# Optimization experiments

Hardware: AMD Instinct MI355X
Metric: run time of the kernel (lower is better)

## Reference

```python
import jax, jax.numpy as jnp
import numpy as np

N, L, C = 4, 1024, 512   # batch, frames, channels (in_channels == mdl_channels)
H = 16                   # heads
D = C // H               # head dim
S = 16                   # number of segments for bi
EPS_PN = 1e-5            # MaskPowerNorm / GroupScaling eps


def setup_inputs() -> dict:
    key = jax.random.key(0)
    ks = jax.random.split(key, 8)
    x = jax.random.normal(ks[0], (N, L, C), jnp.float32)
    bi = jnp.sort(jax.random.randint(ks[1], (L,), 0, S)).astype(jnp.int64)
    w_qkv = jax.random.normal(ks[2], (3 * C, C), jnp.float32) * 0.02
    w_beta = jax.random.normal(ks[3], (1, 3 * C), jnp.float32) * 0.02
    w1 = jax.random.normal(ks[4], (C, C), jnp.float32) * 0.02
    b1 = jnp.zeros((C,), jnp.float32)
    w2 = jax.random.normal(ks[5], (C, C), jnp.float32) * 0.02
    b2 = jnp.zeros((C,), jnp.float32)
    pn1_w = jnp.ones((C,), jnp.float32)
    pn1_b = jnp.zeros((C,), jnp.float32)
    pn1_phi = jnp.ones((C,), jnp.float32)
    pn2_w = jnp.ones((C,), jnp.float32)
    pn2_b = jnp.zeros((C,), jnp.float32)
    pn2_phi = jnp.ones((C,), jnp.float32)
    return dict(x=x, bi=bi, w_qkv=w_qkv, w_beta=w_beta, w1=w1, b1=b1, w2=w2,
                b2=b2, pn1_w=pn1_w, pn1_b=pn1_b, pn1_phi=pn1_phi,
                pn2_w=pn2_w, pn2_b=pn2_b, pn2_phi=pn2_phi)


def power_norm(x, weight, bias, running_phi):
    # MaskPowerNorm (eval): GroupScaling1D over H channel groups, then
    # x / sqrt(running_phi + eps) * weight + bias
    n, l, c = x.shape
    cg = c // H
    g = x.reshape(n, l, H, cg)
    m2 = jnp.mean(g * g, axis=-1, keepdims=True)
    gs = (g / jnp.sqrt(m2 + EPS_PN)).reshape(n, l, c)
    return gs / jnp.sqrt(running_phi + EPS_PN) * weight + bias


def reference(x, bi, w_qkv, w_beta, w1, b1, w2, b2,
              pn1_w, pn1_b, pn1_phi, pn2_w, pn2_b, pn2_phi):
    n, l, c = x.shape
    d = c // H
    # QKV projection (bias=False)
    qkv = x @ w_qkv.T                                  # (n, l, 3c)
    q, k, v = jnp.split(qkv, 3, axis=-1)
    q = q.reshape(n, l, H, d)
    k = k.reshape(n, l, H, d)
    v = v.reshape(n, l, H, d)
    # elu feature map on temperature-scaled q, k
    temp = d ** (-0.25)
    phi = lambda t: jax.nn.elu(t * temp) + 1.0
    q = phi(q).transpose(0, 2, 1, 3)                   # (n, h, l, d)
    k = phi(k).transpose(0, 2, 1, 3)                   # (n, h, l, d)
    vt = v.transpose(0, 2, 1, 3)                       # (n, h, l, d)
    # per-position outer products k v^T : (n, h, l, d, d)
    kv = k[..., :, None] * vt[..., None, :]
    # scatter_sum over frames into S segments, then gather back per frame
    kv_seg = jnp.zeros((n, H, S, d, d), kv.dtype).at[:, :, bi].add(kv)
    kv_g = kv_seg[:, :, bi]                            # (n, h, l, d, d)
    k_seg = jnp.zeros((n, H, S, d), k.dtype).at[:, :, bi].add(k)
    k_g = k_seg[:, :, bi]                              # (n, h, l, d)
    z = 1.0 / jnp.sum(q * k_g, axis=-1)                # (n, h, l)
    v_out = jnp.einsum('nhld,nhldm->nhlm', q, kv_g) * z[..., None]
    t = v_out.transpose(0, 2, 1, 3).reshape(n, l, c)   # (n, l, c)
    # AddNorm with beta gate (dropout is identity in eval)
    beta = jax.nn.sigmoid(jnp.concatenate([t, x, t - x], axis=-1) @ w_beta.T)
    x1 = power_norm(beta * x + (1.0 - beta) * t, pn1_w, pn1_b, pn1_phi)
    # FFN (exact GELU) + AddNorm (no beta)
    ff = jax.nn.gelu(x1 @ w1.T + b1, approximate=False) @ w2.T + b2
    return power_norm(ff + x1, pn2_w, pn2_b, pn2_phi)
```

## Files before the change

### kernel.cpp

```cpp
#include <hip/hip_runtime.h>
#include <math.h>

#define NB 4
#define LB 1024
#define CB 512
#define HH 16
#define DD 32
#define SS 16
#define NL (NB*LB)
#define C3 (3*CB)

typedef __attribute__((ext_vector_type(8))) short short8;
typedef __attribute__((ext_vector_type(4))) float f32x4;

__device__ __forceinline__ unsigned short f2bf_rn(float f) {
  unsigned u = __builtin_bit_cast(unsigned, f);
  unsigned r = u + 0x7FFFu + ((u >> 16) & 1u);
  return (unsigned short)(r >> 16);
}
__device__ __forceinline__ float bf2f(unsigned short h) {
  unsigned u = ((unsigned)h) << 16;
  return __builtin_bit_cast(float, u);
}

__device__ __forceinline__ int lower_bound_i32(const int* a, int n, int v) {
  int lo = 0, hi = n;
  while (lo < hi) { int mid = (lo + hi) >> 1; if (a[mid] < v) lo = mid + 1; else hi = mid; }
  return lo;
}

template<int MODE, int BN>
__global__ __launch_bounds__(256) void gemm_mfma(
    const float* __restrict__ A, const float* __restrict__ B, float* __restrict__ Co,
    int M, int Nn, int K,
    const float* __restrict__ bias, const float* __restrict__ res)
{
  constexpr int NJ = BN / 32;
  __shared__ short8 Ah8[4*128], Al8[4*128];
  __shared__ short8 Bh8[4*BN],  Bl8[4*BN];
  const int tid  = threadIdx.x;
  const int lane = tid & 63, wave = tid >> 6;
  const int wm = wave >> 1, wn = wave & 1;
  const int l15 = lane & 15, l4 = lane >> 4;
  const int bm = blockIdx.x * 128, bn = blockIdx.y * BN;

  f32x4 acc[4][NJ];
  #pragma unroll
  for (int i = 0; i < 4; ++i)
    #pragma unroll
    for (int j = 0; j < NJ; ++j)
      acc[i][j] = {0.f, 0.f, 0.f, 0.f};

  const int arow = tid >> 1, ah2 = tid & 1;
  const float* Ag = A + (long)(bm + arow) * K + ah2 * 16;
  const int brow128 = tid >> 1, bh2 = tid & 1;
  const int brow64  = tid >> 2, bq  = tid & 3;
  const float* Bg = (BN == 128) ? (B + (long)(bn + brow128) * K + bh2 * 16)
                                : (B + (long)(bn + brow64)  * K + bq * 8);

  for (int k0 = 0; k0 < K; k0 += 32) {
    if (k0) __syncthreads();
    {
      const float4* g = (const float4*)(Ag + k0);
      const float4 q0 = g[0], q1 = g[1], q2 = g[2], q3 = g[3];
      const float f[16] = {q0.x,q0.y,q0.z,q0.w, q1.x,q1.y,q1.z,q1.w,
                           q2.x,q2.y,q2.z,q2.w, q3.x,q3.y,q3.z,q3.w};
      #pragma unroll
      for (int cc = 0; cc < 2; ++cc) {
        short8 hi, lo;
        #pragma unroll
        for (int e = 0; e < 8; ++e) {
          const float v = f[cc*8 + e];
          const unsigned short hb = f2bf_rn(v);
          hi[e] = (short)hb;
          lo[e] = (short)f2bf_rn(v - bf2f(hb));
        }
        const int idx = (ah2*2 + cc)*128 + arow;
        Ah8[idx] = hi; Al8[idx] = lo;
      }
    }
    if (BN == 128) {
      const float4* g = (const float4*)(Bg + k0);
      const float4 q0 = g[0], q1 = g[1], q2 = g[2], q3 = g[3];
      const float f[16] = {q0.x,q0.y,q0.z,q0.w, q1.x,q1.y,q1.z,q1.w,
                           q2.x,q2.y,q2.z,q2.w, q3.x,q3.y,q3.z,q3.w};
      #pragma unroll
      for (int cc = 0; cc < 2; ++cc) {
        short8 hi, lo;
        #pragma unroll
        for (int e = 0; e < 8; ++e) {
          const float v = f[cc*8 + e];
          const unsigned short hb = f2bf_rn(v);
          hi[e] = (short)hb;
          lo[e] = (short)f2bf_rn(v - bf2f(hb));
        }
        const int idx = (bh2*2 + cc)*BN + brow128;
        Bh8[idx] = hi; Bl8[idx] = lo;
      }
    } else {
      const float4* g = (const float4*)(Bg + k0);
      const float4 q0 = g[0], q1 = g[1];
      const float f[8] = {q0.x,q0.y,q0.z,q0.w, q1.x,q1.y,q1.z,q1.w};
      short8 hi, lo;
      #pragma unroll
      for (int e = 0; e < 8; ++e) {
        const float v = f[e];
        const unsigned short hb = f2bf_rn(v);
        hi[e] = (short)hb;
        lo[e] = (short)f2bf_rn(v - bf2f(hb));
      }
      const int idx = bq*BN + brow64;
      Bh8[idx] = hi; Bl8[idx] = lo;
    }
    __syncthreads();

    short8 bhf[NJ], blf[NJ];
    #pragma unroll
    for (int j = 0; j < NJ; ++j) {
      const int idx = l4*BN + wn*(NJ*16) + j*16 + l15;
      bhf[j] = Bh8[idx]; blf[j] = Bl8[idx];
    }
    #pragma unroll
    for (int i = 0; i < 4; ++i) {
      const int idx = l4*128 + wm*64 + i*16 + l15;
      const short8 ah = Ah8[idx], al = Al8[idx];
      #pragma unroll
      for (int j = 0; j < NJ; ++j) {
        acc[i][j] = __builtin_amdgcn_mfma_f32_16x16x32_bf16(ah, bhf[j], acc[i][j], 0, 0, 0);
        acc[i][j] = __builtin_amdgcn_mfma_f32_16x16x32_bf16(ah, blf[j], acc[i][j], 0, 0, 0);
        acc[i][j] = __builtin_amdgcn_mfma_f32_16x16x32_bf16(al, bhf[j], acc[i][j], 0, 0, 0);
      }
    }
  }

  const float temp = 0.42044820762685725f;
  #pragma unroll
  for (int i = 0; i < 4; ++i) {
    #pragma unroll
    for (int j = 0; j < NJ; ++j) {
      const int n  = bn + wn*(NJ*16) + j*16 + l15;
      const int mb = bm + wm*64 + i*16 + l4*4;
      #pragma unroll
      for (int r = 0; r < 4; ++r) {
        const int m = mb + r;
        float v = acc[i][j][r];
        if (MODE == 0) {
          if (n < 2*CB) { const float z = v * temp; v = (z > 0.f) ? (z + 1.f) : expf(z); }
        } else if (MODE == 1) {
          v += bias[n];
          v = v * 0.5f * (1.f + erff(v * 0.70710678118654752f));
        } else {
          v += bias[n] + res[(long)m * Nn + n];
        }
        Co[(long)m * Nn + n] = v;
      }
    }
  }
}

__global__ __launch_bounds__(256) void seg_sums(
    const float* __restrict__ qkv, const int* __restrict__ bi,
    float* __restrict__ segkv, float* __restrict__ segk)
{
  const int b = blockIdx.x;
  const int s = b & (SS-1);
  const int h = (b >> 4) & (HH-1);
  const int n = b >> 8;
  __shared__ int sb[2];
  __shared__ float ks[8][DD];
  __shared__ float vs[8][DD];
  const int tid = threadIdx.x;
  if (tid == 0) {
    sb[0] = lower_bound_i32(bi, LB, s);
    sb[1] = lower_bound_i32(bi, LB, s + 1);
  }
  __syncthreads();
  const int lo = sb[0], hi = sb[1];
  const int li = tid >> 5, c = tid & 31;
  const int d  = tid >> 3, m0 = (tid & 7) * 4;
  float a0=0.f,a1=0.f,a2=0.f,a3=0.f, ksum=0.f;
  for (int l0 = lo; l0 < hi; l0 += 8) {
    const int l = l0 + li;
    __syncthreads();
    if (l < hi) {
      const float* row = qkv + (long)(n*LB + l) * C3;
      ks[li][c] = row[CB   + h*DD + c];
      vs[li][c] = row[2*CB + h*DD + c];
    } else {
      ks[li][c] = 0.f; vs[li][c] = 0.f;
    }
    __syncthreads();
    #pragma unroll
    for (int q = 0; q < 8; ++q) {
      const float kd = ks[q][d];
      ksum += kd;
      a0 = fmaf(kd, vs[q][m0+0], a0);
      a1 = fmaf(kd, vs[q][m0+1], a1);
      a2 = fmaf(kd, vs[q][m0+2], a2);
      a3 = fmaf(kd, vs[q][m0+3], a3);
    }
  }
  *(float4*)&segkv[(long)b*(DD*DD) + d*DD + m0] = make_float4(a0,a1,a2,a3);
  if ((tid & 7) == 0) segk[b*DD + d] = ksum;
}

__global__ __launch_bounds__(256) void seg_vout(
    const float* __restrict__ qkv, const int* __restrict__ bi,
    const float* __restrict__ segkv, const float* __restrict__ segk,
    float* __restrict__ tbuf)
{
  const int b = blockIdx.x;
  const int s = b & (SS-1);
  const int h = (b >> 4) & (HH-1);
  const int n = b >> 8;
  __shared__ float KVs[DD*DD];
  __shared__ float Ks[DD];
  __shared__ float qs[8][DD];
  __shared__ int sb[2];
  const int tid = threadIdx.x;
  if (tid == 0) {
    sb[0] = lower_bound_i32(bi, LB, s);
    sb[1] = lower_bound_i32(bi, LB, s + 1);
  }
  #pragma unroll
  for (int i = 0; i < 4; ++i) KVs[tid + i*256] = segkv[(long)b*(DD*DD) + tid + i*256];
  if (tid < DD) Ks[tid] = segk[b*DD + tid];
  __syncthreads();
  const int lo = sb[0], hi = sb[1];
  const int li = tid >> 5, m = tid & 31;
  for (int l0 = lo; l0 < hi; l0 += 8) {
    const int l = l0 + li;
    __syncthreads();
    if (l < hi) qs[li][m] = qkv[(long)(n*LB + l) * C3 + h*DD + m];
    __syncthreads();
    if (l < hi) {
      float vo = 0.f, den = 0.f;
      #pragma unroll
      for (int d2 = 0; d2 < DD; ++d2) {
        const float qd = qs[li][d2];
        vo  = fmaf(qd, KVs[d2*DD + m], vo);
        den = fmaf(qd, Ks[d2], den);
      }
      tbuf[(long)(n*LB + l) * CB + h*DD + m] = vo / den;
    }
  }
}

__global__ __launch_bounds__(256) void beta_pn1(
    const float* __restrict__ x, const float* __restrict__ tbuf,
    const float* __restrict__ w_beta,
    const float* __restrict__ pw, const float* __restrict__ pb, const float* __restrict__ pphi,
    float* __restrict__ x1)
{
  const int row = blockIdx.x;
  const int tid = threadIdx.x;
  const int c0 = tid * 2;
  const long base = (long)row * CB;
  const float2 xv = *(const float2*)&x[base + c0];
  const float2 tv = *(const float2*)&tbuf[base + c0];
  float p = tv.x * w_beta[c0]   + xv.x * w_beta[CB + c0]   + (tv.x - xv.x) * w_beta[2*CB + c0]
          + tv.y * w_beta[c0+1] + xv.y * w_beta[CB + c0+1] + (tv.y - xv.y) * w_beta[2*CB + c0+1];
  #pragma unroll
  for (int off = 32; off >= 1; off >>= 1) p += __shfl_xor(p, off, 64);
  __shared__ float red[4];
  if ((tid & 63) == 0) red[tid >> 6] = p;
  __syncthreads();
  const float zsum = red[0] + red[1] + red[2] + red[3];
  const float beta = 1.f / (1.f + expf(-zsum));
  const float y0 = beta * xv.x + (1.f - beta) * tv.x;
  const float y1 = beta * xv.y + (1.f - beta) * tv.y;
  float ss = y0*y0 + y1*y1;
  #pragma unroll
  for (int off = 1; off < 16; off <<= 1) ss += __shfl_xor(ss, off, 64);
  const float inv = rsqrtf(ss * (1.f/32.f) + 1e-5f);
  const float o0 = y0 * inv * rsqrtf(pphi[c0]   + 1e-5f) * pw[c0]   + pb[c0];
  const float o1 = y1 * inv * rsqrtf(pphi[c0+1] + 1e-5f) * pw[c0+1] + pb[c0+1];
  *(float2*)&x1[base + c0] = make_float2(o0, o1);
}

__global__ __launch_bounds__(256) void pn2_kernel(
    const float* __restrict__ ffx,
    const float* __restrict__ pw, const float* __restrict__ pb, const float* __restrict__ pphi,
    float* __restrict__ out)
{
  const int row = blockIdx.x;
  const int tid = threadIdx.x;
  const int c0 = tid * 2;
  const long base = (long)row * CB;
  const float2 yv = *(const float2*)&ffx[base + c0];
  float ss = yv.x*yv.x + yv.y*yv.y;
  #pragma unroll
  for (int off = 1; off < 16; off <<= 1) ss += __shfl_xor(ss, off, 64);
  const float inv = rsqrtf(ss * (1.f/32.f) + 1e-5f);
  const float o0 = yv.x * inv * rsqrtf(pphi[c0]   + 1e-5f) * pw[c0]   + pb[c0];
  const float o1 = yv.y * inv * rsqrtf(pphi[c0+1] + 1e-5f) * pw[c0+1] + pb[c0+1];
  *(float2*)&out[base + c0] = make_float2(o0, o1);
}

extern "C" void kernel_launch(void* const* d_in, const int* in_sizes, int n_in,
                              void* d_out, int out_size, void* d_ws, size_t ws_size,
                              hipStream_t stream)
{
  const float* x       = (const float*)d_in[0];
  const int*   bi      = (const int*)d_in[1];
  const float* w_qkv   = (const float*)d_in[2];
  const float* w_beta  = (const float*)d_in[3];
  const float* w1      = (const float*)d_in[4];
  const float* b1      = (const float*)d_in[5];
  const float* w2      = (const float*)d_in[6];
  const float* b2      = (const float*)d_in[7];
  const float* pn1_w   = (const float*)d_in[8];
  const float* pn1_b   = (const float*)d_in[9];
  const float* pn1_phi = (const float*)d_in[10];
  const float* pn2_w   = (const float*)d_in[11];
  const float* pn2_b   = (const float*)d_in[12];
  const float* pn2_phi = (const float*)d_in[13];
  float* out = (float*)d_out;
  float* ws  = (float*)d_ws;

  float* qkv   = ws;
  float* segkv = qkv + (long)NL*C3;
  float* segk  = segkv + (long)NB*HH*SS*DD*DD;
  float* tbuf  = segk + (long)NB*HH*SS*DD;
  float* x1    = tbuf + (long)NL*CB;
  float* h1    = qkv;
  float* ffx   = qkv + (long)NL*CB;

  gemm_mfma<0,128><<<dim3(NL/128, C3/128), 256, 0, stream>>>(x,  w_qkv, qkv, NL, C3, CB, nullptr, nullptr);
  seg_sums  <<<NB*HH*SS, 256, 0, stream>>>(qkv, bi, segkv, segk);
  seg_vout  <<<NB*HH*SS, 256, 0, stream>>>(qkv, bi, segkv, segk, tbuf);
  beta_pn1  <<<NL, 256, 0, stream>>>(x, tbuf, w_beta, pn1_w, pn1_b, pn1_phi, x1);
  gemm_mfma<1,64><<<dim3(NL/128, CB/64), 256, 0, stream>>>(x1, w1, h1,  NL, CB, CB, b1, nullptr);
  gemm_mfma<2,64><<<dim3(NL/128, CB/64), 256, 0, stream>>>(h1, w2, ffx, NL, CB, CB, b2, x1);
  pn2_kernel<<<NL, 256, 0, stream>>>(ffx, pn2_w, pn2_b, pn2_phi, out);
}
```

Measured before the change: 228.1 us.

## Pre-split operands to bf16 hi/lo and load GEMM tiles via global_load_lds

```diff
diff --git a/kernel.cpp b/kernel.cpp
--- a/kernel.cpp
+++ b/kernel.cpp
@@ -13,6 +13,10 @@
 typedef __attribute__((ext_vector_type(8))) short short8;
 typedef __attribute__((ext_vector_type(4))) float f32x4;
 
+#define GL16(gp, lp) __builtin_amdgcn_global_load_lds( \
+    (const __attribute__((address_space(1))) void*)(gp), \
+    (__attribute__((address_space(3))) void*)(lp), 16, 0, 0)
+
 __device__ __forceinline__ unsigned short f2bf_rn(float f) {
   unsigned u = __builtin_bit_cast(unsigned, f);
   unsigned r = u + 0x7FFFu + ((u >> 16) & 1u);
@@ -29,19 +33,51 @@
   return lo;
 }
 
+#define X4T   524288
+#define WQ4T  720896
+#define W14T  786432
+#define TOT4  851968
+__global__ __launch_bounds__(256) void split_conv(
+    const float* __restrict__ x, const float* __restrict__ wqkv,
+    const float* __restrict__ w1, const float* __restrict__ w2,
+    ushort* __restrict__ xh, ushort* __restrict__ xl,
+    ushort* __restrict__ wqh, ushort* __restrict__ wql,
+    ushort* __restrict__ w1h, ushort* __restrict__ w1l,
+    ushort* __restrict__ w2h, ushort* __restrict__ w2l)
+{
+  for (int idx = blockIdx.x * 256 + threadIdx.x; idx < TOT4; idx += gridDim.x * 256) {
+    const float* src; ushort *dh, *dl; int off;
+    if (idx < X4T)        { src = x;    dh = xh;  dl = xl;  off = idx; }
+    else if (idx < WQ4T)  { src = wqkv; dh = wqh; dl = wql; off = idx - X4T; }
+    else if (idx < W14T)  { src = w1;   dh = w1h; dl = w1l; off = idx - WQ4T; }
+    else                  { src = w2;   dh = w2h; dl = w2l; off = idx - W14T; }
+    const float4 v = ((const float4*)src)[off];
+    ushort4 h, l;
+    h.x = f2bf_rn(v.x); l.x = f2bf_rn(v.x - bf2f(h.x));
+    h.y = f2bf_rn(v.y); l.y = f2bf_rn(v.y - bf2f(h.y));
+    h.z = f2bf_rn(v.z); l.z = f2bf_rn(v.z - bf2f(h.z));
+    h.w = f2bf_rn(v.w); l.w = f2bf_rn(v.w - bf2f(h.w));
+    ((ushort4*)dh)[off] = h;
+    ((ushort4*)dl)[off] = l;
+  }
+}
+
 template<int MODE, int BN>
-__global__ __launch_bounds__(256) void gemm_mfma(
-    const float* __restrict__ A, const float* __restrict__ B, float* __restrict__ Co,
+__global__ __launch_bounds__(256) void gemm_mfma2(
+    const ushort* __restrict__ Ah, const ushort* __restrict__ Al,
+    const ushort* __restrict__ Bh, const ushort* __restrict__ Bl,
     int M, int Nn, int K,
-    const float* __restrict__ bias, const float* __restrict__ res)
+    const float* __restrict__ bias,
+    float* __restrict__ Cf, ushort* __restrict__ Ch, ushort* __restrict__ Cl,
+    const ushort* __restrict__ resh, const ushort* __restrict__ resl)
 {
   constexpr int NJ = BN / 32;
-  __shared__ short8 Ah8[4*128], Al8[4*128];
-  __shared__ short8 Bh8[4*BN],  Bl8[4*BN];
-  const int tid  = threadIdx.x;
-  const int lane = tid & 63, wave = tid >> 6;
-  const int wm = wave >> 1, wn = wave & 1;
-  const int l15 = lane & 15, l4 = lane >> 4;
+  __shared__ short8 AhL[512], AlL[512];
+  __shared__ short8 BhL[4*BN], BlL[4*BN];
+  const int tid = threadIdx.x;
+  const int w = tid >> 6, l = tid & 63;
+  const int wm = w >> 1, wn = w & 1;
+  const int l15 = l & 15, l4 = l >> 4;
   const int bm = blockIdx.x * 128, bn = blockIdx.y * BN;
 
   f32x4 acc[4][NJ];
@@ -51,79 +87,44 @@
     for (int j = 0; j < NJ; ++j)
       acc[i][j] = {0.f, 0.f, 0.f, 0.f};
 
-  const int arow = tid >> 1, ah2 = tid & 1;
-  const float* Ag = A + (long)(bm + arow) * K + ah2 * 16;
-  const int brow128 = tid >> 1, bh2 = tid & 1;
-  const int brow64  = tid >> 2, bq  = tid & 3;
-  const float* Bg = (BN == 128) ? (B + (long)(bn + brow128) * K + bh2 * 16)
-                                : (B + (long)(bn + brow64)  * K + bq * 8);
-
   for (int k0 = 0; k0 < K; k0 += 32) {
     if (k0) __syncthreads();
-    {
-      const float4* g = (const float4*)(Ag + k0);
-      const float4 q0 = g[0], q1 = g[1], q2 = g[2], q3 = g[3];
-      const float f[16] = {q0.x,q0.y,q0.z,q0.w, q1.x,q1.y,q1.z,q1.w,
-                           q2.x,q2.y,q2.z,q2.w, q3.x,q3.y,q3.z,q3.w};
+    #pragma unroll
+    for (int i = 0; i < 2; ++i) {
+      const int pb = i * 256 + w * 64;
+      const int p  = pb + l;
+      const long go = (long)(bm + (p & 127)) * K + k0 + (p >> 7) * 8;
+      GL16(Ah + go, (char*)AhL + pb * 16);
+      GL16(Al + go, (char*)AlL + pb * 16);
+    }
+    if (BN == 128) {
       #pragma unroll
-      for (int cc = 0; cc < 2; ++cc) {
-        short8 hi, lo;
-        #pragma unroll
-        for (int e = 0; e < 8; ++e) {
-          const float v = f[cc*8 + e];
-          const unsigned short hb = f2bf_rn(v);
-          hi[e] = (short)hb;
-          lo[e] = (short)f2bf_rn(v - bf2f(hb));
-        }
-        const int idx = (ah2*2 + cc)*128 + arow;
-        Ah8[idx] = hi; Al8[idx] = lo;
-      }
-    }
-    if (BN == 128) {
-      const float4* g = (const float4*)(Bg + k0);
-      const float4 q0 = g[0], q1 = g[1], q2 = g[2], q3 = g[3];
-      const float f[16] = {q0.x,q0.y,q0.z,q0.w, q1.x,q1.y,q1.z,q1.w,
-                           q2.x,q2.y,q2.z,q2.w, q3.x,q3.y,q3.z,q3.w};
-      #pragma unroll
-      for (int cc = 0; cc < 2; ++cc) {
-        short8 hi, lo;
-        #pragma unroll
-        for (int e = 0; e < 8; ++e) {
-          const float v = f[cc*8 + e];
-          const unsigned short hb = f2bf_rn(v);
-          hi[e] = (short)hb;
-          lo[e] = (short)f2bf_rn(v - bf2f(hb));
-        }
-        const int idx = (bh2*2 + cc)*BN + brow128;
-        Bh8[idx] = hi; Bl8[idx] = lo;
+      for (int i = 0; i < 2; ++i) {
+        const int pb = i * 256 + w * 64;
+        const int p  = pb + l;
+        const long go = (long)(bn + (p & 127)) * K + k0 + (p >> 7) * 8;
+        GL16(Bh + go, (char*)BhL + pb * 16);
+        GL16(Bl + go, (char*)BlL + pb * 16);
       }
     } else {
-      const float4* g = (const float4*)(Bg + k0);
-      const float4 q0 = g[0], q1 = g[1];
-      const float f[8] = {q0.x,q0.y,q0.z,q0.w, q1.x,q1.y,q1.z,q1.w};
-      short8 hi, lo;
-      #pragma unroll
-      for (int e = 0; e < 8; ++e) {
-        const float v = f[e];
-        const unsigned short hb = f2bf_rn(v);
-        hi[e] = (short)hb;
-        lo[e] = (short)f2bf_rn(v - bf2f(hb));
-      }
-      const int idx = bq*BN + brow64;
-      Bh8[idx] = hi; Bl8[idx] = lo;
+      const int pb = w * 64;
+      const int p  = pb + l;
+      const long go = (long)(bn + (p & 63)) * K + k0 + (p >> 6) * 8;
+      GL16(Bh + go, (char*)BhL + pb * 16);
+      GL16(Bl + go, (char*)BlL + pb * 16);
     }
     __syncthreads();
 
     short8 bhf[NJ], blf[NJ];
     #pragma unroll
     for (int j = 0; j < NJ; ++j) {
-      const int idx = l4*BN + wn*(NJ*16) + j*16 + l15;
-      bhf[j] = Bh8[idx]; blf[j] = Bl8[idx];
+      const int idx = l4 * BN + wn * (NJ * 16) + j * 16 + l15;
+      bhf[j] = BhL[idx]; blf[j] = BlL[idx];
     }
     #pragma unroll
     for (int i = 0; i < 4; ++i) {
-      const int idx = l4*128 + wm*64 + i*16 + l15;
-      const short8 ah = Ah8[idx], al = Al8[idx];
+      const int idx = l4 * 128 + wm * 64 + i * 16 + l15;
+      const short8 ah = AhL[idx], al = AlL[idx];
       #pragma unroll
       for (int j = 0; j < NJ; ++j) {
         acc[i][j] = __builtin_amdgcn_mfma_f32_16x16x32_bf16(ah, bhf[j], acc[i][j], 0, 0, 0);
@@ -138,111 +139,105 @@
   for (int i = 0; i < 4; ++i) {
     #pragma unroll
     for (int j = 0; j < NJ; ++j) {
-      const int n  = bn + wn*(NJ*16) + j*16 + l15;
-      const int mb = bm + wm*64 + i*16 + l4*4;
+      const int n  = bn + wn * (NJ * 16) + j * 16 + l15;
+      const int mb = bm + wm * 64 + i * 16 + l4 * 4;
       #pragma unroll
       for (int r = 0; r < 4; ++r) {
         const int m = mb + r;
         float v = acc[i][j][r];
         if (MODE == 0) {
-          if (n < 2*CB) { const float z = v * temp; v = (z > 0.f) ? (z + 1.f) : expf(z); }
+          if (n < 2 * CB) { const float z = v * temp; v = (z > 0.f) ? (z + 1.f) : expf(z); }
+          Cf[(long)m * Nn + n] = v;
         } else if (MODE == 1) {
           v += bias[n];
           v = v * 0.5f * (1.f + erff(v * 0.70710678118654752f));
+          const ushort hb = f2bf_rn(v);
+          Ch[(long)m * Nn + n] = hb;
+          Cl[(long)m * Nn + n] = f2bf_rn(v - bf2f(hb));
         } else {
-          v += bias[n] + res[(long)m * Nn + n];
+          const long o = (long)m * Nn + n;
+          v += bias[n] + bf2f(resh[o]) + bf2f(resl[o]);
+          Cf[o] = v;
         }
-        Co[(long)m * Nn + n] = v;
       }
     }
   }
 }
 
-__global__ __launch_bounds__(256) void seg_sums(
+__global__ __launch_bounds__(256) void seg_attn(
     const float* __restrict__ qkv, const int* __restrict__ bi,
-    float* __restrict__ segkv, float* __restrict__ segk)
+    float* __restrict__ tbuf)
 {
   const int b = blockIdx.x;
   const int s = b & (SS-1);
   const int h = (b >> 4) & (HH-1);
   const int n = b >> 8;
-  __shared__ int sb[2];
-  __shared__ float ks[8][DD];
-  __shared__ float vs[8][DD];
-  const int tid = threadIdx.x;
-  if (tid == 0) {
-    sb[0] = lower_bound_i32(bi, LB, s);
-    sb[1] = lower_bound_i32(bi, LB, s + 1);
-  }
-  __syncthreads();
-  const int lo = sb[0], hi = sb[1];
-  const int li = tid >> 5, c = tid & 31;
-  const int d  = tid >> 3, m0 = (tid & 7) * 4;
-  float a0=0.f,a1=0.f,a2=0.f,a3=0.f, ksum=0.f;
-  for (int l0 = lo; l0 < hi; l0 += 8) {
-    const int l = l0 + li;
-    __syncthreads();
-    if (l < hi) {
-      const float* row = qkv + (long)(n*LB + l) * C3;
-      ks[li][c] = row[CB   + h*DD + c];
-      vs[li][c] = row[2*CB + h*DD + c];
-    } else {
-      ks[li][c] = 0.f; vs[li][c] = 0.f;
-    }
-    __syncthreads();
-    #pragma unroll
-    for (int q = 0; q < 8; ++q) {
-      const float kd = ks[q][d];
-      ksum += kd;
-      a0 = fmaf(kd, vs[q][m0+0], a0);
-      a1 = fmaf(kd, vs[q][m0+1], a1);
-      a2 = fmaf(kd, vs[q][m0+2], a2);
-      a3 = fmaf(kd, vs[q][m0+3], a3);
-    }
-  }
-  *(float4*)&segkv[(long)b*(DD*DD) + d*DD + m0] = make_float4(a0,a1,a2,a3);
-  if ((tid & 7) == 0) segk[b*DD + d] = ksum;
-}
-
-__global__ __launch_bounds__(256) void seg_vout(
-    const float* __restrict__ qkv, const int* __restrict__ bi,
-    const float* __restrict__ segkv, const float* __restrict__ segk,
-    float* __restrict__ tbuf)
-{
-  const int b = blockIdx.x;
-  const int s = b & (SS-1);
-  const int h = (b >> 4) & (HH-1);
-  const int n = b >> 8;
-  __shared__ float KVs[DD*DD];
+  __shared__ float ks[32][DD];
+  __shared__ float vs[32][DD];
+  __shared__ float KVs[DD][DD];
   __shared__ float Ks[DD];
-  __shared__ float qs[8][DD];
   __shared__ int sb[2];
   const int tid = threadIdx.x;
   if (tid == 0) {
     sb[0] = lower_bound_i32(bi, LB, s);
     sb[1] = lower_bound_i32(bi, LB, s + 1);
   }
-  #pragma unroll
-  for (int i = 0; i < 4; ++i) KVs[tid + i*256] = segkv[(long)b*(DD*DD) + tid + i*256];
-  if (tid < DD) Ks[tid] = segk[b*DD + tid];
   __syncthreads();
   const int lo = sb[0], hi = sb[1];
-  const int li = tid >> 5, m = tid & 31;
-  for (int l0 = lo; l0 < hi; l0 += 8) {
-    const int l = l0 + li;
-    __syncthreads();
-    if (l < hi) qs[li][m] = qkv[(long)(n*LB + l) * C3 + h*DD + m];
-    __syncthreads();
-    if (l < hi) {
-      float vo = 0.f, den = 0.f;
-      #pragma unroll
-      for (int d2 = 0; d2 < DD; ++d2) {
-        const float qd = qs[li][d2];
-        vo  = fmaf(qd, KVs[d2*DD + m], vo);
-        den = fmaf(qd, Ks[d2], den);
+  const int srow = tid >> 3, sq = tid & 7;
+  const int d = tid >> 3, m0 = (tid & 7) * 4;
+  float4 acc = make_float4(0.f, 0.f, 0.f, 0.f);
+  float ksum = 0.f;
+
+  for (int l0 = lo; l0 < hi; l0 += 32) {
+    const int lr = l0 + srow;
+    if (lr < hi) {
+      const float* row = qkv + (long)(n*LB + lr) * C3 + h*DD;
+      *(float4*)&ks[srow][sq*4] = *(const float4*)(row + CB   + sq*4);
+      *(float4*)&vs[srow][sq*4] = *(const float4*)(row + 2*CB + sq*4);
+    } else {
+      *(float4*)&ks[srow][sq*4] = make_float4(0.f,0.f,0.f,0.f);
+      *(float4*)&vs[srow][sq*4] = make_float4(0.f,0.f,0.f,0.f);
+    }
+    __syncthreads();
+    #pragma unroll
+    for (int r = 0; r < 32; ++r) {
+      const float kd = ks[r][d];
+      ksum += kd;
+      const float4 vv = *(const float4*)&vs[r][m0];
+      acc.x = fmaf(kd, vv.x, acc.x);
+      acc.y = fmaf(kd, vv.y, acc.y);
+      acc.z = fmaf(kd, vv.z, acc.z);
+      acc.w = fmaf(kd, vv.w, acc.w);
+    }
+    __syncthreads();
+  }
+  *(float4*)&KVs[d][m0] = acc;
+  if ((tid & 7) == 0) Ks[d] = ksum;
+  __syncthreads();
+
+  const int prow = tid >> 5, m = tid & 31;
+  for (int l0 = lo; l0 < hi; l0 += 32) {
+    const int lr = l0 + srow;
+    if (lr < hi)
+      *(float4*)&ks[srow][sq*4] = *(const float4*)(qkv + (long)(n*LB + lr) * C3 + h*DD + sq*4);
+    __syncthreads();
+    #pragma unroll
+    for (int step = 0; step < 4; ++step) {
+      const int r  = step * 8 + prow;
+      const int l2 = l0 + r;
+      if (l2 < hi) {
+        float vo = 0.f, den = 0.f;
+        #pragma unroll
+        for (int d2 = 0; d2 < DD; ++d2) {
+          const float qd = ks[r][d2];
+          vo  = fmaf(qd, KVs[d2][m], vo);
+          den = fmaf(qd, Ks[d2], den);
+        }
+        tbuf[(long)(n*LB + l2) * CB + h*DD + m] = vo / den;
       }
-      tbuf[(long)(n*LB + l) * CB + h*DD + m] = vo / den;
-    }
+    }
+    __syncthreads();
   }
 }
 
@@ -250,7 +245,7 @@
     const float* __restrict__ x, const float* __restrict__ tbuf,
     const float* __restrict__ w_beta,
     const float* __restrict__ pw, const float* __restrict__ pb, const float* __restrict__ pphi,
-    float* __restrict__ x1)
+    ushort* __restrict__ x1h, ushort* __restrict__ x1l)
 {
   const int row = blockIdx.x;
   const int tid = threadIdx.x;
@@ -275,7 +270,10 @@
   const float inv = rsqrtf(ss * (1.f/32.f) + 1e-5f);
   const float o0 = y0 * inv * rsqrtf(pphi[c0]   + 1e-5f) * pw[c0]   + pb[c0];
   const float o1 = y1 * inv * rsqrtf(pphi[c0+1] + 1e-5f) * pw[c0+1] + pb[c0+1];
-  *(float2*)&x1[base + c0] = make_float2(o0, o1);
+  const ushort h0 = f2bf_rn(o0), h1 = f2bf_rn(o1);
+  const ushort g0 = f2bf_rn(o0 - bf2f(h0)), g1 = f2bf_rn(o1 - bf2f(h1));
+  *(ushort2*)&x1h[base + c0] = make_ushort2(h0, h1);
+  *(ushort2*)&x1l[base + c0] = make_ushort2(g0, g1);
 }
 
 __global__ __launch_bounds__(256) void pn2_kernel(
@@ -316,21 +314,33 @@
   const float* pn2_b   = (const float*)d_in[12];
   const float* pn2_phi = (const float*)d_in[13];
   float* out = (float*)d_out;
-  float* ws  = (float*)d_ws;
-
-  float* qkv   = ws;
-  float* segkv = qkv + (long)NL*C3;
-  float* segk  = segkv + (long)NB*HH*SS*DD*DD;
-  float* tbuf  = segk + (long)NB*HH*SS*DD;
-  float* x1    = tbuf + (long)NL*CB;
-  float* h1    = qkv;
-  float* ffx   = qkv + (long)NL*CB;
-
-  gemm_mfma<0,128><<<dim3(NL/128, C3/128), 256, 0, stream>>>(x,  w_qkv, qkv, NL, C3, CB, nullptr, nullptr);
-  seg_sums  <<<NB*HH*SS, 256, 0, stream>>>(qkv, bi, segkv, segk);
-  seg_vout  <<<NB*HH*SS, 256, 0, stream>>>(qkv, bi, segkv, segk, tbuf);
-  beta_pn1  <<<NL, 256, 0, stream>>>(x, tbuf, w_beta, pn1_w, pn1_b, pn1_phi, x1);
-  gemm_mfma<1,64><<<dim3(NL/128, CB/64), 256, 0, stream>>>(x1, w1, h1,  NL, CB, CB, b1, nullptr);
-  gemm_mfma<2,64><<<dim3(NL/128, CB/64), 256, 0, stream>>>(h1, w2, ffx, NL, CB, CB, b2, x1);
+  char*  wsb = (char*)d_ws;
+
+  ushort* wqh  = (ushort*)(wsb);
+  ushort* wql  = (ushort*)(wsb +  1572864);
+  ushort* w1h  = (ushort*)(wsb +  3145728);
+  ushort* w1l  = (ushort*)(wsb +  3670016);
+  ushort* w2h  = (ushort*)(wsb +  4194304);
+  ushort* w2l  = (ushort*)(wsb +  4718592);
+  ushort* xh   = (ushort*)(wsb +  5242880);
+  ushort* xl   = (ushort*)(wsb +  9437184);
+  float*  tbuf = (float*) (wsb +  5242880);
+  float*  qkvb = (float*) (wsb + 13631488);
+  ushort* x1h  = (ushort*)(wsb + 13631488);
+  ushort* x1l  = (ushort*)(wsb + 17825792);
+  ushort* h1h  = (ushort*)(wsb + 22020096);
+  ushort* h1l  = (ushort*)(wsb + 26214400);
+  float*  ffx  = (float*) (wsb + 30408704);
+
+  split_conv<<<2048, 256, 0, stream>>>(x, w_qkv, w1, w2,
+                                       xh, xl, wqh, wql, w1h, w1l, w2h, w2l);
+  gemm_mfma2<0,128><<<dim3(NL/128, C3/128), 256, 0, stream>>>(
+      xh, xl, wqh, wql, NL, C3, CB, nullptr, qkvb, nullptr, nullptr, nullptr, nullptr);
+  seg_attn<<<NB*HH*SS, 256, 0, stream>>>(qkvb, bi, tbuf);
+  beta_pn1<<<NL, 256, 0, stream>>>(x, tbuf, w_beta, pn1_w, pn1_b, pn1_phi, x1h, x1l);
+  gemm_mfma2<1,64><<<dim3(NL/128, CB/64), 256, 0, stream>>>(
+      x1h, x1l, w1h, w1l, NL, CB, CB, b1, nullptr, h1h, h1l, nullptr, nullptr);
+  gemm_mfma2<2,64><<<dim3(NL/128, CB/64), 256, 0, stream>>>(
+      h1h, h1l, w2h, w2l, NL, CB, CB, b2, ffx, nullptr, nullptr, x1h, x1l);
   pn2_kernel<<<NL, 256, 0, stream>>>(ffx, pn2_w, pn2_b, pn2_phi, out);
 }
```

Result: faster. 223.4 us (-2.0%).
